# Optimization experiments

Measured on AMD Instinct MI355X. Metric: run time of the kernel, lower is better.

## Reference

```python
import jax, jax.numpy as jnp
import numpy as np

K = 16  # kNN neighbors (KnnEncoder default)


def _bn(h, g, s):
    # eval-mode BatchNorm with running mean 0 / var 1 folded into affine
    return h * g + s


def setup_inputs() -> dict:
    key = jax.random.key(0)
    cnt = [0]
    def nk():
        cnt[0] += 1
        return jax.random.fold_in(key, cnt[0])
    B, N = 4, 4096
    def W(i, o):
        return jax.random.normal(nk(), (i, o), jnp.float32) / np.float32(i) ** 0.5
    def bias(d):
        return jnp.zeros((d,), jnp.float32)
    def gamma(d):
        return jnp.ones((d,), jnp.float32) + 0.1 * jax.random.normal(nk(), (d,), jnp.float32)
    def beta(d):
        return 0.1 * jax.random.normal(nk(), (d,), jnp.float32)
    inp = dict(
        pos=jax.random.normal(nk(), (B, N, 3), jnp.float32),
        query_point_idx=jax.random.randint(nk(), (B,), 0, N),
        # PointNetConv local MLP: 6 -> 64 -> 128 -> 256 (plain last)
        cw1=W(6, 64), cb1=bias(64), cg1=gamma(64), cs1=beta(64),
        cw2=W(64, 128), cb2=bias(128), cg2=gamma(128), cs2=beta(128),
        cw3=W(128, 256), cb3=bias(256),
        # GlobalSAModule MLP: 259 -> 256 -> 512 -> 1024 (plain last)
        sw1=W(259, 256), sb1=bias(256), sg1=gamma(256), ss1=beta(256),
        sw2=W(256, 512), sb2=bias(512), sg2=gamma(512), ss2=beta(512),
        sw3=W(512, 1024), sb3=bias(1024),
        # EdgeGraspPredictor: 1280 -> 512 -> 256 -> 16
        pw1=W(1280, 512), pb1=bias(512),
        pw2=W(512, 256), pb2=bias(256),
        pw3=W(256, 16), pb3=bias(16),
    )
    return inp


def reference(pos, query_point_idx, cw1, cb1, cg1, cs1, cw2, cb2, cg2, cs2, cw3, cb3,
              sw1, sb1, sg1, ss1, sw2, sb2, sg2, ss2, sw3, sb3,
              pw1, pb1, pw2, pb2, pw3, pb3):
    B, N, _ = pos.shape
    # kNN within each cloud (self included, as torch_geometric knn with x==y)
    d2 = jnp.sum((pos[:, :, None, :] - pos[:, None, :, :]) ** 2, axis=-1)  # [B,N,N]
    _, idx = jax.lax.top_k(-d2, K)  # [B,N,K] targets for each source point n
    nbr = jax.vmap(lambda p, i: p[i])(pos, idx)  # [B,N,K,3] target positions
    # PointNetConv message: cat([x_j = pos_src, pos_src - pos_tgt])
    src = jnp.broadcast_to(pos[:, :, None, :], (B, N, K, 3))
    h = jnp.concatenate([src, src - nbr], axis=-1)  # [B,N,K,6]
    h = jnp.maximum(_bn(h @ cw1 + cb1, cg1, cs1), 0.0)
    h = jnp.maximum(_bn(h @ cw2 + cb2, cg2, cs2), 0.0)
    m = h @ cw3 + cb3  # [B,N,K,256] per-edge messages
    # scatter-max aggregation at target nodes (every node has its self edge)
    tgt = (idx + (jnp.arange(B) * N)[:, None, None]).reshape(-1)
    x = jax.ops.segment_max(m.reshape(-1, m.shape[-1]), tgt, num_segments=B * N)
    x = x.reshape(B, N, -1)  # [B,N,256] per-point features
    # GlobalSAModule: pointwise MLP then global max pool per cloud
    g = jnp.concatenate([x, pos], axis=-1)  # [B,N,259]
    g = jnp.maximum(_bn(g @ sw1 + sb1, sg1, ss1), 0.0)
    g = jnp.maximum(_bn(g @ sw2 + sb2, sg2, ss2), 0.0)
    g = g @ sw3 + sb3  # [B,N,1024]
    scene = jnp.max(g, axis=1)  # [B,1024]
    # gather query point feature, concat with scene feature, predictor MLP
    q = query_point_idx + jnp.arange(B) * N
    point_feat = x.reshape(B * N, -1)[q]  # [B,256]
    ef = jnp.concatenate([point_feat, scene], axis=-1)  # [B,1280]
    h = jnp.maximum(ef @ pw1 + pb1, 0.0)
    h = jnp.maximum(h @ pw2 + pb2, 0.0)
    return h @ pw3 + pb3  # [B,16]
```

## Files before the change

### kernel.cpp

```cpp
#include <hip/hip_runtime.h>

#define BB 4
#define NN 4096
#define KK 16

typedef unsigned short u16;
typedef unsigned int   u32;
typedef unsigned long long u64;

typedef __attribute__((ext_vector_type(8))) short bf16x8;
typedef __attribute__((ext_vector_type(4))) float f32x4;

__device__ __forceinline__ float b2f(u16 x){ return __uint_as_float(((u32)x) << 16); }
__device__ __forceinline__ u16 f2b(float f){
    u32 u = __float_as_uint(f);
    u32 r = (u + 0x7FFFu + ((u >> 16) & 1u)) >> 16;
    return (u16)r;
}
__device__ __forceinline__ u32 fmap(float f){
    u32 u = __float_as_uint(f);
    return (u & 0x80000000u) ? ~u : (u | 0x80000000u);
}
__device__ __forceinline__ float funmap(u32 u){
    u32 v = (u & 0x80000000u) ? (u ^ 0x80000000u) : ~u;
    return __uint_as_float(v);
}

#define N_ARR 27
__device__ const int ASZ[N_ARR] = {
    49152, 384, 64, 64, 64, 8192, 128, 128, 128, 32768, 256,
    66304, 256, 256, 256, 131072, 512, 512, 512, 524288, 1024,
    655360, 512, 131072, 256, 4096, 16 };
__device__ const int AOFF[N_ARR] = {
    0, 49152, 49536, 49600, 49664, 49728, 57920, 58048, 58176, 58304, 91072,
    91328, 157632, 157888, 158144, 158400, 289472, 289984, 290496, 291008, 815296,
    816320, 1471680, 1472192, 1603264, 1603520, 1607616 };

struct Ptrs { const void* p[N_ARR]; };

#define O_POS 0
#define O_CW1 49152
#define O_CB1 49536
#define O_CG1 49600
#define O_CS1 49664
#define O_CW2 49728
#define O_CB2 57920
#define O_CG2 58048
#define O_CS2 58176
#define O_CW3 58304
#define O_CB3 91072
#define O_SW1 91328
#define O_SB1 157632
#define O_SG1 157888
#define O_SS1 158144
#define O_SW2 158400
#define O_SB2 289472
#define O_SG2 289984
#define O_SS2 290496
#define O_SW3 291008
#define O_SB3 815296
#define O_PW1 816320
#define O_PB1 1471680
#define O_PW2 1472192
#define O_PB2 1603264
#define O_PW3 1603520
#define O_PB3 1607616

__global__ void detect_kernel(const u16* __restrict__ pos_u16, u32* __restrict__ flag){
    __shared__ int cnt;
    if (threadIdx.x == 0) cnt = 0;
    __syncthreads();
    int c = 0;
    #pragma unroll
    for (int s = 0; s < 4; ++s){
        u16 u = pos_u16[2*(threadIdx.x*4 + s)];
        int e = (u >> 7) & 0xFF;
        c += (e >= 0x68 && e <= 0x82) ? 1 : 0;
    }
    atomicAdd(&cnt, c);
    __syncthreads();
    if (threadIdx.x == 0) *flag = (cnt >= 512) ? 1u : 0u;
}

__device__ __forceinline__ void pack_one_src(const void* __restrict__ src, bool isbf,
                                             u16* __restrict__ dst, int tot, int log2n,
                                             int g, int T){
    const int nmask = (1 << log2n) - 1;
    for (int id = g; id < tot; id += T){
        int i = id & 7, lg = (id >> 3) & 3;
        int rest = id >> 5;
        int n = rest & nmask;
        int ks = rest >> log2n;
        int si = (ks*32 + lg*8 + i) << log2n | n;
        dst[id] = isbf ? ((const u16*)src)[si] : f2b(((const float*)src)[si]);
    }
}

__global__ __launch_bounds__(256) void prep_kernel(Ptrs pt, const u32* __restrict__ flagp,
        float* __restrict__ dst,
        u16* __restrict__ wp2, u16* __restrict__ wp3,
        u16* __restrict__ swp1, u16* __restrict__ swp2, u16* __restrict__ swp3){
    const bool isbf = (*flagp != 0);
    const int T = gridDim.x * 256;
    const int g = blockIdx.x * 256 + threadIdx.x;
    #pragma unroll
    for (int a = 0; a < N_ARR; ++a){
        const int sz = ASZ[a], off = AOFF[a];
        if (isbf){
            const u16* s = (const u16*)pt.p[a];
            for (int i = g; i < sz; i += T) dst[off + i] = b2f(s[i]);
        } else {
            const float* s = (const float*)pt.p[a];
            for (int i = g; i < sz; i += T) dst[off + i] = s[i];
        }
    }
    pack_one_src(pt.p[5],  isbf, wp2,    8192,  7, g, T);
    pack_one_src(pt.p[9],  isbf, wp3,   32768,  8, g, T);
    pack_one_src(pt.p[11], isbf, swp1,  65536,  8, g, T);
    pack_one_src(pt.p[15], isbf, swp2, 131072,  9, g, T);
    pack_one_src(pt.p[19], isbf, swp3, 524288, 10, g, T);
}

__global__ __launch_bounds__(256) void knn_kernel(const float* __restrict__ conv,
                                                  int* __restrict__ knn_out,
                                                  u32* __restrict__ deg){
    __shared__ float sx[NN], sy[NN], sz[NN];
    const float* posf = conv + O_POS;
    const int b  = blockIdx.x >> 10;
    const int i0 = (blockIdx.x & 1023) << 2;
    const int tid = threadIdx.x;
    for (int t = tid; t < NN; t += 256){
        const float* p = posf + ((size_t)(b*NN + t))*3;
        sx[t] = p[0]; sy[t] = p[1]; sz[t] = p[2];
    }
    __syncthreads();
    const int lane = tid & 63;
    const int i = i0 + (tid >> 6);
    const float pix = sx[i], piy = sy[i], piz = sz[i];

    float d[KK]; int id[KK];
    #pragma unroll
    for (int t = 0; t < KK; ++t){
        int j = lane + (t << 6);
        float dx = pix - sx[j], dy = piy - sy[j], dz = piz - sz[j];
        d[t] = __fadd_rn(__fadd_rn(__fmul_rn(dx,dx), __fmul_rn(dy,dy)), __fmul_rn(dz,dz));
        id[t] = j;
    }
    float dmax = d[0]; int amax = 0;
    #pragma unroll
    for (int p = 1; p < KK; ++p){ bool c = d[p] > dmax; dmax = c ? d[p] : dmax; amax = c ? p : amax; }

    for (int t = KK; t < 64; ++t){
        int j = lane + (t << 6);
        float dx = pix - sx[j], dy = piy - sy[j], dz = piz - sz[j];
        float d2 = __fadd_rn(__fadd_rn(__fmul_rn(dx,dx), __fmul_rn(dy,dy)), __fmul_rn(dz,dz));
        if (d2 < dmax){
            #pragma unroll
            for (int p = 0; p < KK; ++p){ bool c = (p == amax); d[p] = c ? d2 : d[p]; id[p] = c ? j : id[p]; }
            dmax = d[0]; amax = 0;
            #pragma unroll
            for (int p = 1; p < KK; ++p){ bool c = d[p] > dmax; dmax = c ? d[p] : dmax; amax = c ? p : amax; }
        }
    }
    u64 key[KK];
    #pragma unroll
    for (int p = 0; p < KK; ++p) key[p] = (((u64)__float_as_uint(d[p])) << 32) | (u32)id[p];
    int* outp = knn_out + ((size_t)(b*NN + i))*KK;
    for (int r = 0; r < KK; ++r){
        u64 m = key[0];
        #pragma unroll
        for (int p = 1; p < KK; ++p) m = key[p] < m ? key[p] : m;
        #pragma unroll
        for (int off = 32; off > 0; off >>= 1){
            u64 o = __shfl_xor(m, off);
            m = o < m ? o : m;
        }
        if (lane == 0){
            int j = (int)(u32)(m & 0xFFFFFFFFu);
            outp[r] = j;
            atomicAdd(deg + (b << 12) + j, 1u);
        }
        #pragma unroll
        for (int p = 0; p < KK; ++p) if (key[p] == m) key[p] = ~0ull;
    }
}

__global__ __launch_bounds__(1024) void scan_kernel(const u32* __restrict__ deg,
                                                    int* __restrict__ rowstart, u32* __restrict__ cursor){
    __shared__ int lsum[1024];
    const int tid = threadIdx.x;
    const int base = tid * 16;
    int loc[16]; int s = 0;
    #pragma unroll
    for (int q = 0; q < 16; ++q){ loc[q] = (int)deg[base+q]; s += loc[q]; }
    lsum[tid] = s;
    __syncthreads();
    int acc = s;
    for (int ofs = 1; ofs < 1024; ofs <<= 1){
        int t = (tid >= ofs) ? lsum[tid-ofs] : 0;
        __syncthreads();
        acc += t; lsum[tid] = acc;
        __syncthreads();
    }
    int excl = acc - s;
    #pragma unroll
    for (int q = 0; q < 16; ++q){
        rowstart[base+q] = excl; cursor[base+q] = (u32)excl; excl += loc[q];
    }
    if (tid == 1023) rowstart[16384] = excl;
}

__global__ __launch_bounds__(256) void fill_kernel(const int* __restrict__ knn,
                                                   u32* __restrict__ cursor, int* __restrict__ csr){
    int e = blockIdx.x*256 + threadIdx.x;
    int b = e >> 16;
    int t = (b << 12) + knn[e];
    u32 pos = atomicAdd(cursor + t, 1u);
    csr[pos] = e;
}

__device__ __forceinline__ bf16x8 ldfrag(const u16* h, int row, int kofs, int rowstride){
    u32 byte = (u32)((row*rowstride + kofs)*2) ^ (u32)((row & 7) << 4);
    return *(const bf16x8*)((const char*)h + byte);
}
__device__ __forceinline__ void st16(u16* h, int row, int col, int rowstride, float v){
    u32 byte = (u32)((row*rowstride + col)*2) ^ (u32)((row & 7) << 4);
    *(u16*)((char*)h + byte) = f2b(v);
}

__global__ __launch_bounds__(256, 2) void edge_kernel(
    const float* __restrict__ conv, const int* __restrict__ knn,
    const int* __restrict__ rowstart, const int* __restrict__ csr,
    const u16* __restrict__ wp2, const u16* __restrict__ wp3,
    u16* __restrict__ xh)
{
    __shared__ float in6[6][64];
    __shared__ int   lts[64];
    __shared__ int   rs_l[17];
    __shared__ float scw1[384];
    __shared__ float sc1[64], sh1[64];
    __shared__ __align__(16) u16 h1s[64*64];
    __shared__ __align__(16) u16 h2s[64*128];
    __shared__ u32 lsx[16*256];

    const float* posf = conv + O_POS;
    const float* cb1 = conv + O_CB1; const float* cg1 = conv + O_CG1; const float* cs1 = conv + O_CS1;

    const int tid = threadIdx.x;
    const int w   = tid >> 6;
    const int l   = tid & 63;
    const int t0  = blockIdx.x << 4;
    const int b   = t0 >> 12;

    if (tid < 64){ float g1 = cg1[tid]; sc1[tid]=g1; sh1[tid]=cb1[tid]*g1 + cs1[tid]; }
    if (tid < 17) rs_l[tid] = rowstart[t0 + tid];
    for (int u = tid; u < 384; u += 256) scw1[u] = conv[O_CW1 + u];
    #pragma unroll
    for (int q = 0; q < 16; ++q) lsx[q*256 + tid] = 0u;

    const int lr = l & 15, lg = l >> 4;
    const int colb2 = w << 5;
    const int colb3 = w << 6;

    float sc2v[2], sh2v[2], bs3v[4];
    #pragma unroll
    for (int nt = 0; nt < 2; ++nt){
        int c = colb2 + nt*16 + lr;
        float g2 = conv[O_CG2 + c];
        sc2v[nt] = g2; sh2v[nt] = conv[O_CB2 + c]*g2 + conv[O_CS2 + c];
    }
    #pragma unroll
    for (int nt = 0; nt < 4; ++nt) bs3v[nt] = conv[O_CB3 + colb3 + nt*16 + lr];

    __syncthreads();
    const int segstart = rs_l[0], segend = rs_l[16];
    const int nchunk = (segend - segstart + 63) >> 6;

    int curl = -1;
    float run[4];
    #pragma unroll
    for (int nt = 0; nt < 4; ++nt) run[nt] = 0.f;

    for (int ch = 0; ch < nchunk; ++ch){
        __syncthreads();
        if (tid < 64){
            int gpos = segstart + (ch << 6) + tid;
            int lt = -1;
            float ax=0,ay=0,az=0,dx=0,dy=0,dz=0;
            if (gpos < segend){
                lt = 0;
                #pragma unroll
                for (int q = 1; q < 16; ++q) lt += (gpos >= rs_l[q]) ? 1 : 0;
                int e = csr[gpos];
                int i = (e >> 4) & (NN - 1);
                int j = knn[e];
                const float* pi = posf + ((size_t)(b*NN + i))*3;
                const float* pj = posf + ((size_t)(b*NN + j))*3;
                ax = pi[0]; ay = pi[1]; az = pi[2];
                dx = ax - pj[0]; dy = ay - pj[1]; dz = az - pj[2];
            }
            lts[tid] = lt;
            in6[0][tid]=ax; in6[1][tid]=ay; in6[2][tid]=az;
            in6[3][tid]=dx; in6[4][tid]=dy; in6[5][tid]=dz;
        }
        __syncthreads();

        {
            const int e = tid & 63, c0g = (tid >> 6) << 4;
            float a0=in6[0][e], a1=in6[1][e], a2=in6[2][e],
                  a3=in6[3][e], a4=in6[4][e], a5=in6[5][e];
            u32 pk[8];
            #pragma unroll
            for (int ci = 0; ci < 16; ++ci){
                int cc = c0g + ci;
                float acc = a0*scw1[cc]     + a1*scw1[64+cc]  + a2*scw1[128+cc]
                          + a3*scw1[192+cc] + a4*scw1[256+cc] + a5*scw1[320+cc];
                float v = fmaxf(acc*sc1[cc] + sh1[cc], 0.f);
                u32 h = (u32)f2b(v);
                if (ci & 1) pk[ci >> 1] |= h << 16; else pk[ci >> 1] = h;
            }
            u32 base = (u32)(e*128 + c0g*2);
            u32 swz  = (u32)((e & 7) << 4);
            *(uint4*)((char*)h1s + (base ^ swz))        = make_uint4(pk[0],pk[1],pk[2],pk[3]);
            *(uint4*)((char*)h1s + ((base + 16) ^ swz)) = make_uint4(pk[4],pk[5],pk[6],pk[7]);
        }
        __syncthreads();

        {
            f32x4 acc2[4][2];
            #pragma unroll
            for (int mt = 0; mt < 4; ++mt)
                #pragma unroll
                for (int nt = 0; nt < 2; ++nt) acc2[mt][nt] = (f32x4){0.f,0.f,0.f,0.f};
            #pragma unroll
            for (int ks = 0; ks < 2; ++ks){
                bf16x8 bf[2];
                #pragma unroll
                for (int nt = 0; nt < 2; ++nt)
                    bf[nt] = *(const bf16x8*)(wp2 + (((ks*128 + colb2 + nt*16 + lr) << 2) + lg)*8);
                #pragma unroll
                for (int mt = 0; mt < 4; ++mt){
                    bf16x8 a = ldfrag(h1s, mt*16 + lr, ks*32 + lg*8, 64);
                    #pragma unroll
                    for (int nt = 0; nt < 2; ++nt)
                        acc2[mt][nt] = __builtin_amdgcn_mfma_f32_16x16x32_bf16(a, bf[nt], acc2[mt][nt], 0, 0, 0);
                }
            }
            #pragma unroll
            for (int mt = 0; mt < 4; ++mt)
                #pragma unroll
                for (int nt = 0; nt < 2; ++nt)
                    #pragma unroll
                    for (int r = 0; r < 4; ++r){
                        int row = mt*16 + lg*4 + r;
                        float v = fmaxf(acc2[mt][nt][r]*sc2v[nt] + sh2v[nt], 0.f);
                        st16(h2s, row, colb2 + nt*16 + lr, 128, v);
                    }
        }
        __syncthreads();

        {
            f32x4 acc3[4][4];
            #pragma unroll
            for (int mt = 0; mt < 4; ++mt)
                #pragma unroll
                for (int nt = 0; nt < 4; ++nt) acc3[mt][nt] = (f32x4){0.f,0.f,0.f,0.f};
            #pragma unroll
            for (int ks = 0; ks < 4; ++ks){
                bf16x8 bf[4];
                #pragma unroll
                for (int nt = 0; nt < 4; ++nt)
                    bf[nt] = *(const bf16x8*)(wp3 + (((ks*256 + colb3 + nt*16 + lr) << 2) + lg)*8);
                #pragma unroll
                for (int mt = 0; mt < 4; ++mt){
                    bf16x8 a = ldfrag(h2s, mt*16 + lr, ks*32 + lg*8, 128);
                    #pragma unroll
                    for (int nt = 0; nt < 4; ++nt)
                        acc3[mt][nt] = __builtin_amdgcn_mfma_f32_16x16x32_bf16(a, bf[nt], acc3[mt][nt], 0, 0, 0);
                }
            }
            #pragma unroll
            for (int mt = 0; mt < 4; ++mt)
                #pragma unroll
                for (int r = 0; r < 4; ++r){
                    int row = mt*16 + lg*4 + r;
                    int lt = lts[row];
                    if (lt != curl){
                        if (curl >= 0){
                            #pragma unroll
                            for (int nt = 0; nt < 4; ++nt)
                                atomicMax(&lsx[curl*256 + colb3 + nt*16 + lr], fmap(run[nt]));
                        }
                        curl = lt;
                        #pragma unroll
                        for (int nt = 0; nt < 4; ++nt) run[nt] = acc3[mt][nt][r] + bs3v[nt];
                    } else {
                        #pragma unroll
                        for (int nt = 0; nt < 4; ++nt) run[nt] = fmaxf(run[nt], acc3[mt][nt][r] + bs3v[nt]);
                    }
                }
        }
    }
    if (curl >= 0){
        #pragma unroll
        for (int nt = 0; nt < 4; ++nt)
            atomicMax(&lsx[curl*256 + colb3 + nt*16 + lr], fmap(run[nt]));
    }
    __syncthreads();
    #pragma unroll
    for (int q = 0; q < 16; ++q)
        xh[((size_t)(t0+q))*256 + tid] = f2b(funmap(lsx[q*256 + tid]));
}

__global__ __launch_bounds__(256, 2) void sa_kernel(
    const float* __restrict__ conv, const u16* __restrict__ xh,
    const u16* __restrict__ swp1, const u16* __restrict__ swp2, const u16* __restrict__ swp3,
    u32* __restrict__ scene_map)
{
    __shared__ __align__(16) u16 a0s[32*256];
    __shared__ __align__(16) u16 h1s[32*256];
    __shared__ __align__(16) u16 h2s[32*512];
    __shared__ float spw[3][256];
    __shared__ float spx[32], spy[32], spz[32];

    const int tid = threadIdx.x;
    const int w   = tid >> 6;
    const int l   = tid & 63;
    const int lr  = l & 15, lg = l >> 4;
    const int b   = blockIdx.x >> 7;
    const int n0  = (blockIdx.x & 127) << 5;

    #pragma unroll
    for (int it = 0; it < 4; ++it){
        int slot = it*256 + tid;
        int row = slot >> 5, ch0 = (slot & 31) << 3;
        uint4 v = *(const uint4*)(xh + ((size_t)(b*NN + n0 + row))*256 + ch0);
        *(uint4*)((char*)a0s + ((u32)(row*512 + ch0*2) ^ (u32)((row & 7) << 4))) = v;
    }
    if (tid < 96){
        int p = tid & 31, d = tid >> 5;
        float v = conv[O_POS + ((size_t)(b*NN + n0 + p))*3 + d];
        if (d == 0) spx[p] = v; else if (d == 1) spy[p] = v; else spz[p] = v;
    }
    for (int u = tid; u < 768; u += 256)
        spw[u >> 8][u & 255] = conv[O_SW1 + (256 + (u >> 8))*256 + (u & 255)];
    __syncthreads();

    {
        const int c0 = w << 6;
        float sc1v[4], sh1v[4];
        #pragma unroll
        for (int nt = 0; nt < 4; ++nt){
            int cc = c0 + nt*16 + lr;
            float g = conv[O_SG1 + cc];
            sc1v[nt] = g; sh1v[nt] = conv[O_SB1 + cc]*g + conv[O_SS1 + cc];
        }
        f32x4 acc[2][4];
        #pragma unroll
        for (int mt = 0; mt < 2; ++mt)
            #pragma unroll
            for (int nt = 0; nt < 4; ++nt)
                #pragma unroll
                for (int r = 0; r < 4; ++r){
                    int row = mt*16 + lg*4 + r;
                    int cc  = c0 + nt*16 + lr;
                    acc[mt][nt][r] = spx[row]*spw[0][cc] + spy[row]*spw[1][cc] + spz[row]*spw[2][cc];
                }
        #pragma unroll
        for (int ks = 0; ks < 8; ++ks){
            bf16x8 bf[4];
            #pragma unroll
            for (int nt = 0; nt < 4; ++nt)
                bf[nt] = *(const bf16x8*)(swp1 + (((ks*256 + c0 + nt*16 + lr) << 2) + lg)*8);
            #pragma unroll
            for (int mt = 0; mt < 2; ++mt){
                bf16x8 a = ldfrag(a0s, mt*16 + lr, ks*32 + lg*8, 256);
                #pragma unroll
                for (int nt = 0; nt < 4; ++nt)
                    acc[mt][nt] = __builtin_amdgcn_mfma_f32_16x16x32_bf16(a, bf[nt], acc[mt][nt], 0, 0, 0);
            }
        }
        #pragma unroll
        for (int mt = 0; mt < 2; ++mt)
            #pragma unroll
            for (int nt = 0; nt < 4; ++nt)
                #pragma unroll
                for (int r = 0; r < 4; ++r){
                    int row = mt*16 + lg*4 + r;
                    float v = fmaxf(acc[mt][nt][r]*sc1v[nt] + sh1v[nt], 0.f);
                    st16(h1s, row, c0 + nt*16 + lr, 256, v);
                }
    }
    __syncthreads();

    {
        const int c0 = w << 7;
        float sc2v[8], sh2v[8];
        #pragma unroll
        for (int nt = 0; nt < 8; ++nt){
            int cc = c0 + nt*16 + lr;
            float g = conv[O_SG2 + cc];
            sc2v[nt] = g; sh2v[nt] = conv[O_SB2 + cc]*g + conv[O_SS2 + cc];
        }
        f32x4 acc[2][8];
        #pragma unroll
        for (int mt = 0; mt < 2; ++mt)
            #pragma unroll
            for (int nt = 0; nt < 8; ++nt) acc[mt][nt] = (f32x4){0.f,0.f,0.f,0.f};
        #pragma unroll
        for (int ks = 0; ks < 8; ++ks){
            bf16x8 bf[8];
            #pragma unroll
            for (int nt = 0; nt < 8; ++nt)
                bf[nt] = *(const bf16x8*)(swp2 + (((ks*512 + c0 + nt*16 + lr) << 2) + lg)*8);
            #pragma unroll
            for (int mt = 0; mt < 2; ++mt){
                bf16x8 a = ldfrag(h1s, mt*16 + lr, ks*32 + lg*8, 256);
                #pragma unroll
                for (int nt = 0; nt < 8; ++nt)
                    acc[mt][nt] = __builtin_amdgcn_mfma_f32_16x16x32_bf16(a, bf[nt], acc[mt][nt], 0, 0, 0);
            }
        }
        #pragma unroll
        for (int mt = 0; mt < 2; ++mt)
            #pragma unroll
            for (int nt = 0; nt < 8; ++nt)
                #pragma unroll
                for (int r = 0; r < 4; ++r){
                    int row = mt*16 + lg*4 + r;
                    float v = fmaxf(acc[mt][nt][r]*sc2v[nt] + sh2v[nt], 0.f);
                    st16(h2s, row, c0 + nt*16 + lr, 512, v);
                }
    }
    __syncthreads();

    #pragma unroll
    for (int half = 0; half < 2; ++half){
        const int c0 = (half << 9) + (w << 7);
        f32x4 acc[2][8];
        #pragma unroll
        for (int mt = 0; mt < 2; ++mt)
            #pragma unroll
            for (int nt = 0; nt < 8; ++nt) acc[mt][nt] = (f32x4){0.f,0.f,0.f,0.f};
        #pragma unroll
        for (int ks = 0; ks < 16; ++ks){
            bf16x8 bf[8];
            #pragma unroll
            for (int nt = 0; nt < 8; ++nt)
                bf[nt] = *(const bf16x8*)(swp3 + (((ks*1024 + c0 + nt*16 + lr) << 2) + lg)*8);
            #pragma unroll
            for (int mt = 0; mt < 2; ++mt){
                bf16x8 a = ldfrag(h2s, mt*16 + lr, ks*32 + lg*8, 512);
                #pragma unroll
                for (int nt = 0; nt < 8; ++nt)
                    acc[mt][nt] = __builtin_amdgcn_mfma_f32_16x16x32_bf16(a, bf[nt], acc[mt][nt], 0, 0, 0);
            }
        }
        #pragma unroll
        for (int nt = 0; nt < 8; ++nt){
            float v = acc[0][nt][0];
            #pragma unroll
            for (int mt = 0; mt < 2; ++mt)
                #pragma unroll
                for (int r = 0; r < 4; ++r) v = fmaxf(v, acc[mt][nt][r]);
            v = fmaxf(v, __shfl_xor(v, 16));
            v = fmaxf(v, __shfl_xor(v, 32));
            if (lg == 0){
                int cc = c0 + nt*16 + lr;
                atomicMax(scene_map + (b << 10) + cc, fmap(v + conv[O_SB3 + cc]));
            }
        }
    }
}

__global__ __launch_bounds__(128) void head1_kernel(
    const float* __restrict__ conv,
    const u16* __restrict__ xh, const u32* __restrict__ scene_map, const int* __restrict__ qidx,
    float* __restrict__ h1out)
{
    __shared__ float ef[1280];
    const float* pw1 = conv + O_PW1; const float* pb1 = conv + O_PB1;
    const int b  = blockIdx.x >> 2;
    const int c0 = (blockIdx.x & 3) << 7;
    const int tid = threadIdx.x;
    const int q = qidx[b];
    for (int u = tid; u < 1280; u += 128){
        float v;
        if (u < 256) v = b2f(xh[(((size_t)(b*NN + q)) << 8) + u]);
        else         v = funmap(scene_map[(b << 10) + (u - 256)]);
        ef[u] = v;
    }
    __syncthreads();
    const int c = c0 + tid;
    float acc = pb1[c];
    for (int r = 0; r < 1280; ++r) acc += ef[r] * pw1[r*512 + c];
    h1out[(b << 9) + c] = fmaxf(acc, 0.f);
}

__global__ __launch_bounds__(256) void head2_kernel(
    const float* __restrict__ conv, const float* __restrict__ h1in,
    const u32* __restrict__ flagp, void* __restrict__ outv)
{
    __shared__ float h1[4][512];
    __shared__ float h2[4][256];
    const float* pw2 = conv + O_PW2; const float* pb2 = conv + O_PB2;
    const float* pw3 = conv + O_PW3; const float* pb3 = conv + O_PB3;
    const int tid = threadIdx.x;
    for (int u = tid; u < 2048; u += 256) h1[u >> 9][u & 511] = h1in[u];
    __syncthreads();
    for (int o = tid; o < 1024; o += 256){
        int b = o >> 8, c = o & 255;
        float acc = pb2[c];
        for (int r = 0; r < 512; ++r) acc += h1[b][r] * pw2[r*256 + c];
        h2[b][c] = fmaxf(acc, 0.f);
    }
    __syncthreads();
    if (tid < 64){
        int b = tid >> 4, c = tid & 15;
        float acc = pb3[c];
        for (int r = 0; r < 256; ++r) acc += h2[b][r] * pw3[r*16 + c];
        if (*flagp) ((u16*)outv)[tid] = f2b(acc);
        else        ((float*)outv)[tid] = acc;
    }
}

extern "C" void kernel_launch(void* const* d_in, const int* in_sizes, int n_in,
                              void* d_out, int out_size, void* d_ws, size_t ws_size,
                              hipStream_t stream){
    (void)in_sizes; (void)n_in; (void)out_size; (void)ws_size;
    const int* qidx = (const int*)d_in[1];

    char* ws = (char*)d_ws;
    u32*  flag      = (u32*)ws;
    float* conv     = (float*)(ws + 1024);
    u16*  wp2       = (u16*)(ws + 6432768);
    u16*  wp3       = (u16*)(ws + 6449152);
    u16*  swp1      = (u16*)(ws + 6514688);
    u16*  swp2      = (u16*)(ws + 6645760);
    u16*  swp3      = (u16*)(ws + 6907904);
    int*  knn       = (int*)(ws + 7956480);
    u32*  deg       = (u32*)(ws + 9005056);
    u32*  scene_map = (u32*)(ws + 9070592);
    int*  rowstart  = (int*)(ws + 9086976);
    u32*  cursor    = (u32*)(ws + 9152576);
    int*  csr       = (int*)(ws + 9218112);
    u16*  xh        = (u16*)(ws + 10266688);
    float* h1ws     = (float*)(ws + 18655296);

    Ptrs pt;
    pt.p[0] = d_in[0];
    for (int k = 1; k < N_ARR; ++k) pt.p[k] = d_in[k + 1];

    hipMemsetAsync(ws + 9005056, 0, 81920, stream);

    detect_kernel <<<1, 256, 0, stream>>>((const u16*)d_in[0], flag);
    prep_kernel   <<<512, 256, 0, stream>>>(pt, flag, conv, wp2, wp3, swp1, swp2, swp3);
    knn_kernel <<<4096, 256, 0, stream>>>(conv, knn, deg);
    scan_kernel<<<1, 1024, 0, stream>>>(deg, rowstart, cursor);
    fill_kernel<<<1024, 256, 0, stream>>>(knn, cursor, csr);
    edge_kernel<<<1024, 256, 0, stream>>>(conv, knn, rowstart, csr, wp2, wp3, xh);
    sa_kernel  <<<512, 256, 0, stream>>>(conv, xh, swp1, swp2, swp3, scene_map);
    head1_kernel<<<16, 128, 0, stream>>>(conv, xh, scene_map, qidx, h1ws);
    head2_kernel<<<1, 256, 0, stream>>>(conv, h1ws, flag, (void*)d_out);
}
```

Measured before the change: 453.8 us.

## Replace per-lane top-16 register lists with wave-shared candidate buffer and threshold refinement

Measured after the change: 395.6 us. 1.15x faster.

```diff
diff --git a/kernel.cpp b/kernel.cpp
--- a/kernel.cpp
+++ b/kernel.cpp
@@ -121,67 +121,80 @@
     pack_one_src(pt.p[19], isbf, swp3, 524288, 10, g, T);
 }
 
-__global__ __launch_bounds__(256) void knn_kernel(const float* __restrict__ conv,
-                                                  int* __restrict__ knn_out,
-                                                  u32* __restrict__ deg){
-    __shared__ float sx[NN], sy[NN], sz[NN];
-    const float* posf = conv + O_POS;
-    const int b  = blockIdx.x >> 10;
-    const int i0 = (blockIdx.x & 1023) << 2;
-    const int tid = threadIdx.x;
-    for (int t = tid; t < NN; t += 256){
-        const float* p = posf + ((size_t)(b*NN + t))*3;
-        sx[t] = p[0]; sy[t] = p[1]; sz[t] = p[2];
-    }
-    __syncthreads();
-    const int lane = tid & 63;
-    const int i = i0 + (tid >> 6);
-    const float pix = sx[i], piy = sy[i], piz = sz[i];
-
-    float d[KK]; int id[KK];
-    #pragma unroll
-    for (int t = 0; t < KK; ++t){
-        int j = lane + (t << 6);
-        float dx = pix - sx[j], dy = piy - sy[j], dz = piz - sz[j];
-        d[t] = __fadd_rn(__fadd_rn(__fmul_rn(dx,dx), __fmul_rn(dy,dy)), __fmul_rn(dz,dz));
-        id[t] = j;
-    }
-    float dmax = d[0]; int amax = 0;
-    #pragma unroll
-    for (int p = 1; p < KK; ++p){ bool c = d[p] > dmax; dmax = c ? d[p] : dmax; amax = c ? p : amax; }
-
-    for (int t = KK; t < 64; ++t){
-        int j = lane + (t << 6);
-        float dx = pix - sx[j], dy = piy - sy[j], dz = piz - sz[j];
-        float d2 = __fadd_rn(__fadd_rn(__fmul_rn(dx,dx), __fmul_rn(dy,dy)), __fmul_rn(dz,dz));
-        if (d2 < dmax){
-            #pragma unroll
-            for (int p = 0; p < KK; ++p){ bool c = (p == amax); d[p] = c ? d2 : d[p]; id[p] = c ? j : id[p]; }
-            dmax = d[0]; amax = 0;
-            #pragma unroll
-            for (int p = 1; p < KK; ++p){ bool c = d[p] > dmax; dmax = c ? d[p] : dmax; amax = c ? p : amax; }
-        }
-    }
-    u64 key[KK];
-    #pragma unroll
-    for (int p = 0; p < KK; ++p) key[p] = (((u64)__float_as_uint(d[p])) << 32) | (u32)id[p];
-    int* outp = knn_out + ((size_t)(b*NN + i))*KK;
+#define QCAP 192
+__device__ __forceinline__ void refine16(u64* __restrict__ buf, int& cnt, float& tau, int lane){
+    u64 loc[3];
+    #pragma unroll
+    for (int q = 0; q < 3; ++q){
+        int p = lane + (q << 6);
+        loc[q] = (p < cnt) ? buf[p] : ~0ull;
+    }
+    u64 m = ~0ull;
+    #pragma unroll
     for (int r = 0; r < KK; ++r){
-        u64 m = key[0];
-        #pragma unroll
-        for (int p = 1; p < KK; ++p) m = key[p] < m ? key[p] : m;
+        m = loc[0];
+        m = loc[1] < m ? loc[1] : m;
+        m = loc[2] < m ? loc[2] : m;
         #pragma unroll
         for (int off = 32; off > 0; off >>= 1){
             u64 o = __shfl_xor(m, off);
             m = o < m ? o : m;
         }
-        if (lane == 0){
-            int j = (int)(u32)(m & 0xFFFFFFFFu);
-            outp[r] = j;
-            atomicAdd(deg + (b << 12) + j, 1u);
-        }
-        #pragma unroll
-        for (int p = 0; p < KK; ++p) if (key[p] == m) key[p] = ~0ull;
+        if (lane == r) buf[r] = m;
+        #pragma unroll
+        for (int q = 0; q < 3; ++q) if (loc[q] == m) loc[q] = ~0ull;
+    }
+    cnt = KK;
+    tau = __uint_as_float((u32)(m >> 32));
+}
+
+__global__ __launch_bounds__(512) void knn_kernel(const float* __restrict__ conv,
+                                                  int* __restrict__ knn_out,
+                                                  u32* __restrict__ deg){
+    __shared__ __align__(16) float sxy[NN*2];
+    __shared__ float szz[NN];
+    __shared__ __align__(16) u64 kbuf[8*QCAP];
+    const float* posf = conv + O_POS;
+    const int b  = blockIdx.x >> 9;
+    const int i0 = (blockIdx.x & 511) << 3;
+    const int tid = threadIdx.x;
+    for (int t = tid; t < NN; t += 512){
+        const float* p = posf + ((size_t)(b*NN + t))*3;
+        sxy[2*t] = p[0]; sxy[2*t+1] = p[1]; szz[t] = p[2];
+    }
+    __syncthreads();
+    const int lane = tid & 63;
+    const int wq = tid >> 6;
+    const int i = i0 + wq;
+    const float pix = sxy[2*i], piy = sxy[2*i+1], piz = szz[i];
+    u64* buf = kbuf + wq*QCAP;
+
+    float tau = 3.0e38f;
+    int cnt = 0;
+    for (int t = 0; t < 64; ++t){
+        int j = lane + (t << 6);
+        float2 xy = *(const float2*)&sxy[2*j];
+        float zz = szz[j];
+        float dx = pix - xy.x, dy = piy - xy.y, dz = piz - zz;
+        float d2 = __fadd_rn(__fadd_rn(__fmul_rn(dx,dx), __fmul_rn(dy,dy)), __fmul_rn(dz,dz));
+        bool push = (d2 <= tau);
+        u64 bal = __ballot(push);
+        if (bal){
+            int nins = __popcll(bal);
+            if (cnt + nins > QCAP) refine16(buf, cnt, tau, lane);
+            if (push){
+                int ofs = __popcll(bal & ((1ull << lane) - 1ull));
+                buf[cnt + ofs] = (((u64)__float_as_uint(d2)) << 32) | (u32)j;
+            }
+            cnt += nins;
+        }
+    }
+    refine16(buf, cnt, tau, lane);
+    if (lane < KK){
+        u64 k = buf[lane];
+        int j = (int)(u32)(k & 0xFFFFFFFFu);
+        knn_out[((size_t)(b*NN + i))*KK + lane] = j;
+        atomicAdd(deg + (b << 12) + j, 1u);
     }
 }
 
@@ -655,7 +668,7 @@
 
     detect_kernel <<<1, 256, 0, stream>>>((const u16*)d_in[0], flag);
     prep_kernel   <<<512, 256, 0, stream>>>(pt, flag, conv, wp2, wp3, swp1, swp2, swp3);
-    knn_kernel <<<4096, 256, 0, stream>>>(conv, knn, deg);
+    knn_kernel <<<2048, 512, 0, stream>>>(conv, knn, deg);
     scan_kernel<<<1, 1024, 0, stream>>>(deg, rowstart, cursor);
     fill_kernel<<<1024, 256, 0, stream>>>(knn, cursor, csr);
     edge_kernel<<<1024, 256, 0, stream>>>(conv, knn, rowstart, csr, wp2, wp3, xh);
```
